# Optimization experiments

Measured on AMD Instinct MI355X. Metric: run time of the kernel, lower is better.

## Reference

```python
import jax, jax.numpy as jnp
import numpy as np

H = 512  # hidden_size

def setup_inputs() -> dict:
    key = jax.random.key(0)
    ks = jax.random.split(key, 5)
    B, S = 2, 512
    feats = jax.random.normal(ks[0], (B, S, H), dtype=jnp.float32)
    # torch Linear init ~ U(-1/sqrt(in), 1/sqrt(in)); scaled normals are fine for a reference
    W1 = jax.random.normal(ks[1], (2 * H, H), dtype=jnp.float32) / np.sqrt(2 * H)
    b1 = jnp.zeros((H,), dtype=jnp.float32)
    W2 = jax.random.normal(ks[2], (H, H // 2), dtype=jnp.float32) / np.sqrt(H)
    b2 = jnp.zeros((H // 2,), dtype=jnp.float32)
    W3 = jax.random.normal(ks[3], (H // 2, 1), dtype=jnp.float32) / np.sqrt(H // 2)
    b3 = jnp.zeros((1,), dtype=jnp.float32)
    return {"features": feats, "W1": W1, "b1": b1, "W2": W2, "b2": b2, "W3": W3, "b3": b3}


def reference(features, W1, b1, W2, b2, W3, b3):
    # cat([f_i, f_j]) @ W1 == f_i @ W1[:H] + f_j @ W1[H:]
    # Precompute the two halves once per residue instead of per pair.
    a = jnp.einsum('bsh,hk->bsk', features, W1[:H])          # [B,S,H]
    c = jnp.einsum('bsh,hk->bsk', features, W1[H:])          # [B,S,H]
    h1 = jax.nn.relu(a[:, :, None, :] + c[:, None, :, :] + b1)  # [B,S,S,H]
    # Dropout(0.1) is identity at inference.
    h2 = jax.nn.relu(jnp.einsum('bijh,hk->bijk', h1, W2) + b2)  # [B,S,S,H//2]
    logits = jnp.einsum('bijk,ko->bijo', h2, W3) + b3            # [B,S,S,1]
    return jax.nn.sigmoid(logits[..., 0])                        # [B,S,S]
```

## Files before the change

kernel.cpp:

```cpp
#include <hip/hip_runtime.h>

#define S_DIM 512
#define H_DIM 512
#define NH 256
#define TI 8
#define TJ 8

#define AS1 __attribute__((address_space(1)))
#define AS3 __attribute__((address_space(3)))

typedef _Float16 half8 __attribute__((ext_vector_type(8)));
typedef _Float16 half4 __attribute__((ext_vector_type(4)));
typedef float f32x4 __attribute__((ext_vector_type(4)));

__device__ __forceinline__ int swz(int r) { return ((r & 1) << 2) | (r >> 1); }

__global__ __launch_bounds__(256) void convert_all_kernel(const float* __restrict__ feats,
        const float* __restrict__ W1, const float* __restrict__ W2,
        _Float16* __restrict__ f16, _Float16* __restrict__ w1L, _Float16* __restrict__ w2L) {
    int blk = blockIdx.x;
    if (blk < 512) {
        int t = blk * 256 + threadIdx.x;
        float4 v = ((const float4*)feats)[t];
        half4 h;
        h.x = (_Float16)v.x; h.y = (_Float16)v.y; h.z = (_Float16)v.z; h.w = (_Float16)v.w;
        ((half4*)f16)[t] = h;
    } else if (blk < 768) {
        int t = (blk - 512) * 256 + threadIdx.x;
        int gcb = t >> 10, n = t & 1023;
        const float* src = (n < H_DIM) ? &W1[(size_t)(gcb * 8) * H_DIM + n]
                                       : &W1[(size_t)(H_DIM + gcb * 8) * H_DIM + (n - H_DIM)];
        half8 v;
#pragma unroll
        for (int j = 0; j < 8; j++) v[j] = (_Float16)src[(size_t)j * H_DIM];
        *(half8*)&w1L[((size_t)gcb * 1024 + n) * 8] = v;
    } else {
        int t = (blk - 768) * 256 + threadIdx.x;
        int gcb = t >> 8, n = t & 255;
        half8 v;
#pragma unroll
        for (int j = 0; j < 8; j++) v[j] = (_Float16)W2[(size_t)(gcb * 8 + j) * NH + n];
        *(half8*)&w2L[((size_t)gcb * 256 + n) * 8] = v;
    }
}

__global__ __launch_bounds__(256) void prep_mfma_kernel(const _Float16* __restrict__ f16,
        const _Float16* __restrict__ w1L, const float* __restrict__ b1,
        _Float16* __restrict__ aH, _Float16* __restrict__ cH) {
    const int n0 = blockIdx.x * 64, m0 = blockIdx.y * 64;
    const int tid = threadIdx.x, wave = tid >> 6, lane = tid & 63;
    const int quad = lane >> 4, l16 = lane & 15;
    const int wm = wave >> 1, wn = wave & 1;
    int mrow[2], ncol[2];
#pragma unroll
    for (int mt = 0; mt < 2; mt++) mrow[mt] = m0 + wm * 32 + mt * 16 + l16;
#pragma unroll
    for (int nt = 0; nt < 2; nt++) ncol[nt] = n0 + wn * 32 + nt * 16 + l16;
    f32x4 acc[2][2];
#pragma unroll
    for (int mt = 0; mt < 2; mt++)
#pragma unroll
        for (int nt = 0; nt < 2; nt++) acc[mt][nt] = (f32x4)0.f;
#pragma unroll
    for (int ks = 0; ks < 16; ks++) {
        int gcb = ks * 4 + quad;
        half8 af[2], bf[2];
#pragma unroll
        for (int mt = 0; mt < 2; mt++)
            af[mt] = *(const half8*)&f16[(size_t)mrow[mt] * H_DIM + gcb * 8];
#pragma unroll
        for (int nt = 0; nt < 2; nt++)
            bf[nt] = *(const half8*)&w1L[((size_t)gcb * 1024 + ncol[nt]) * 8];
#pragma unroll
        for (int nt = 0; nt < 2; nt++)
#pragma unroll
            for (int mt = 0; mt < 2; mt++)
                acc[mt][nt] = __builtin_amdgcn_mfma_f32_16x16x32_f16(af[mt], bf[nt],
                                                                     acc[mt][nt], 0, 0, 0);
    }
    const bool first_half = (n0 < H_DIM);
#pragma unroll
    for (int nt = 0; nt < 2; nt++) {
        float bias = first_half ? b1[ncol[nt]] : 0.f;
#pragma unroll
        for (int mt = 0; mt < 2; mt++)
#pragma unroll
            for (int r = 0; r < 4; r++) {
                int m = m0 + wm * 32 + mt * 16 + quad * 4 + r;
                float v = acc[mt][nt][r] + bias;
                if (first_half) aH[(size_t)m * H_DIM + ncol[nt]] = (_Float16)v;
                else            cH[(size_t)m * H_DIM + (ncol[nt] - H_DIM)] = (_Float16)v;
            }
    }
}

__global__ __launch_bounds__(256, 4) void pair_kernel(
        const _Float16* __restrict__ aH, const _Float16* __restrict__ cH,
        const _Float16* __restrict__ w2L,
        const float* __restrict__ b2, const float* __restrict__ W3,
        const float* __restrict__ b3, float* __restrict__ out) {
    const int jt = blockIdx.x, it = blockIdx.y, b = blockIdx.z;
    const int i0 = it * TI, j0 = jt * TJ;

    __shared__ __align__(16) _Float16 sa[TI * H_DIM];
    __shared__ __align__(16) _Float16 sc[TJ * H_DIM];
    __shared__ __align__(16) _Float16 afb[2][2][4][512];
    __shared__ float spart[4][64];

    const int tid = threadIdx.x;
    const int wave = tid >> 6, lane = tid & 63;
    const int quad = lane >> 4, l16 = lane & 15;
    const int nb = wave * 64;

#pragma unroll
    for (int rr0 = 0; rr0 < 2; rr0++) {
        int rr = rr0 * 4 + wave;
        int gc = lane ^ swz(rr & 7);
        __builtin_amdgcn_global_load_lds(
            (const AS1 unsigned int*)&aH[((size_t)(b * S_DIM + i0 + rr)) * H_DIM + gc * 8],
            (AS3 unsigned int*)&sa[rr * H_DIM], 16, 0, 0);
        __builtin_amdgcn_global_load_lds(
            (const AS1 unsigned int*)&cH[((size_t)(b * S_DIM + j0 + rr)) * H_DIM + gc * 8],
            (AS3 unsigned int*)&sc[rr * H_DIM], 16, 0, 0);
    }

    const int hl = l16 >> 3;
    const int ilW = wave * 2 + hl;
    const int saoffW = ilW * H_DIM;
    const int swzAW = swz(ilW);
    const int jl = l16 & 7;
    const int scoff = jl * H_DIM, swzC = swz(jl);

    f32x4 acc[4][4];
#pragma unroll
    for (int mt = 0; mt < 4; mt++)
#pragma unroll
        for (int nt = 0; nt < 4; nt++) acc[mt][nt] = (f32x4)0.f;

    const _Float16* bp = &w2L[((size_t)quad * 256 + nb + l16) * 8];

    half8 bnxt[4];
#pragma unroll
    for (int nt = 0; nt < 4; nt++) bnxt[nt] = *(const half8*)&bp[nt * 16 * 8];

    __syncthreads();

#pragma unroll
    for (int s = 0; s < 2; s++) {
        const int gcb = s * 4 + quad;
        half8 va = *(const half8*)&sa[saoffW + ((gcb ^ swzAW) * 8)];
        half8 vc = *(const half8*)&sc[scoff + ((gcb ^ swzC) * 8)];
        half8 af = __builtin_elementwise_max(va + vc, (half8)(_Float16)0.f);
        *(half8*)&afb[0][s][wave][lane * 8] = af;
    }
    asm volatile("s_waitcnt lgkmcnt(0)" ::: "memory");
    __builtin_amdgcn_s_barrier();
    __builtin_amdgcn_sched_barrier(0);

#pragma unroll
    for (int e = 0; e < 8; e++) {
        const int buf = e & 1;
#pragma unroll
        for (int s = 0; s < 2; s++) {
            const int ks = e * 2 + s;
            half8 bf[4];
#pragma unroll
            for (int nt = 0; nt < 4; nt++) bf[nt] = bnxt[nt];
            if (ks < 15) {
                const _Float16* bn = bp + (size_t)4 * 256 * 8;
#pragma unroll
                for (int nt = 0; nt < 4; nt++) bnxt[nt] = *(const half8*)&bn[nt * 16 * 8];
                bp = bn;
            }
            if (e < 7) {
                const int gcb = (2 * (e + 1) + s) * 4 + quad;
                half8 va = *(const half8*)&sa[saoffW + ((gcb ^ swzAW) * 8)];
                half8 vc = *(const half8*)&sc[scoff + ((gcb ^ swzC) * 8)];
                half8 af = __builtin_elementwise_max(va + vc, (half8)(_Float16)0.f);
                *(half8*)&afb[buf ^ 1][s][wave][lane * 8] = af;
            }
            half8 afr[4];
#pragma unroll
            for (int mt = 0; mt < 4; mt++)
                afr[mt] = *(const half8*)&afb[buf][s][mt][lane * 8];
            __builtin_amdgcn_s_setprio(1);
#pragma unroll
            for (int nt = 0; nt < 4; nt++)
#pragma unroll
                for (int mt = 0; mt < 4; mt++)
                    acc[mt][nt] = __builtin_amdgcn_mfma_f32_16x16x32_f16(afr[mt], bf[nt],
                                                                         acc[mt][nt], 0, 0, 0);
            __builtin_amdgcn_s_setprio(0);
        }
        if (e < 7) {
            asm volatile("s_waitcnt lgkmcnt(0)" ::: "memory");
            __builtin_amdgcn_s_barrier();
            __builtin_amdgcn_sched_barrier(0);
        }
    }

    float b2v[4], w3v[4];
#pragma unroll
    for (int nt = 0; nt < 4; nt++) {
        int n = nb + nt * 16 + l16;
        b2v[nt] = b2[n];
        w3v[nt] = W3[n];
    }
    float ps[4][4];
#pragma unroll
    for (int mt = 0; mt < 4; mt++)
#pragma unroll
        for (int r = 0; r < 4; r++) {
            float s = 0.f;
#pragma unroll
            for (int nt = 0; nt < 4; nt++) {
                float v = acc[mt][nt][r] + b2v[nt];
                v = v > 0.f ? v : 0.f;
                s += v * w3v[nt];
            }
            ps[mt][r] = s;
        }
#pragma unroll
    for (int mt = 0; mt < 4; mt++)
#pragma unroll
        for (int r = 0; r < 4; r++) {
            float s = ps[mt][r];
            s += __shfl_xor(s, 8, 16);
            s += __shfl_xor(s, 4, 16);
            s += __shfl_xor(s, 2, 16);
            s += __shfl_xor(s, 1, 16);
            ps[mt][r] = s;
        }
    if (l16 == 0) {
#pragma unroll
        for (int mt = 0; mt < 4; mt++)
#pragma unroll
            for (int r = 0; r < 4; r++)
                spart[wave][mt * 16 + quad * 4 + r] = ps[mt][r];
    }
    __syncthreads();
    if (tid < 64) {
        float tot = spart[0][tid] + spart[1][tid] + spart[2][tid] + spart[3][tid] + b3[0];
        float sg = 1.f / (1.f + __expf(-tot));
        int i = i0 + (tid >> 3), j = j0 + (tid & 7);
        out[(size_t)b * S_DIM * S_DIM + (size_t)i * S_DIM + j] = sg;
    }
}

extern "C" void kernel_launch(void* const* d_in, const int* in_sizes, int n_in,
                              void* d_out, int out_size, void* d_ws, size_t ws_size,
                              hipStream_t stream) {
    const float* feats = (const float*)d_in[0];
    const float* W1 = (const float*)d_in[1];
    const float* b1 = (const float*)d_in[2];
    const float* W2 = (const float*)d_in[3];
    const float* b2 = (const float*)d_in[4];
    const float* W3 = (const float*)d_in[5];
    const float* b3 = (const float*)d_in[6];
    float* out = (float*)d_out;

    const int B = in_sizes[0] / (S_DIM * H_DIM);
    const int M = B * S_DIM;

    char* ws = (char*)d_ws;
    _Float16* f16  = (_Float16*)ws;
    _Float16* aH   = (_Float16*)(ws + (1 << 20));
    _Float16* cH   = (_Float16*)(ws + (2 << 20));
    _Float16* w1L  = (_Float16*)(ws + (3 << 20));
    _Float16* w2L  = (_Float16*)(ws + (4 << 20));

    convert_all_kernel<<<832, 256, 0, stream>>>(feats, W1, W2, f16, w1L, w2L);
    prep_mfma_kernel<<<dim3(16, M / 64), 256, 0, stream>>>(f16, w1L, b1, aH, cH);
    pair_kernel<<<dim3(S_DIM / TJ, S_DIM / TI, B), 256, 0, stream>>>(aH, cH, w2L, b2, W3, b3, out);
}
```

Before: 203.9 us.

## Fuse three kernels into one persistent kernel with software grid barriers

Merges the convert, first-layer GEMM and pair kernels into a single persistent kernel of 768 blocks. The stages are separated by atomic-counter grid barriers, and the pair tiles are processed in a grid-stride loop. This is meant to remove two kernel launch gaps and their tail effects. In exchange it adds a memset, two grid-wide spins, and an occupancy hint lowered to 3, and the barrier relies on all 768 blocks being co-resident, which risks deadlock. The persistent loop also loses per-block scheduling flexibility.

```diff
diff --git a/kernel.cpp b/kernel.cpp
--- a/kernel.cpp
+++ b/kernel.cpp
@@ -5,6 +5,7 @@
 #define NH 256
 #define TI 8
 #define TJ 8
+#define NBLK 768
 
 #define AS1 __attribute__((address_space(1)))
 #define AS3 __attribute__((address_space(3)))
@@ -15,92 +16,27 @@
 
 __device__ __forceinline__ int swz(int r) { return ((r & 1) << 2) | (r >> 1); }
 
-__global__ __launch_bounds__(256) void convert_all_kernel(const float* __restrict__ feats,
-        const float* __restrict__ W1, const float* __restrict__ W2,
-        _Float16* __restrict__ f16, _Float16* __restrict__ w1L, _Float16* __restrict__ w2L) {
-    int blk = blockIdx.x;
-    if (blk < 512) {
-        int t = blk * 256 + threadIdx.x;
-        float4 v = ((const float4*)feats)[t];
-        half4 h;
-        h.x = (_Float16)v.x; h.y = (_Float16)v.y; h.z = (_Float16)v.z; h.w = (_Float16)v.w;
-        ((half4*)f16)[t] = h;
-    } else if (blk < 768) {
-        int t = (blk - 512) * 256 + threadIdx.x;
-        int gcb = t >> 10, n = t & 1023;
-        const float* src = (n < H_DIM) ? &W1[(size_t)(gcb * 8) * H_DIM + n]
-                                       : &W1[(size_t)(H_DIM + gcb * 8) * H_DIM + (n - H_DIM)];
-        half8 v;
-#pragma unroll
-        for (int j = 0; j < 8; j++) v[j] = (_Float16)src[(size_t)j * H_DIM];
-        *(half8*)&w1L[((size_t)gcb * 1024 + n) * 8] = v;
-    } else {
-        int t = (blk - 768) * 256 + threadIdx.x;
-        int gcb = t >> 8, n = t & 255;
-        half8 v;
-#pragma unroll
-        for (int j = 0; j < 8; j++) v[j] = (_Float16)W2[(size_t)(gcb * 8 + j) * NH + n];
-        *(half8*)&w2L[((size_t)gcb * 256 + n) * 8] = v;
-    }
+__device__ __forceinline__ void grid_barrier(unsigned* cnt) {
+    __syncthreads();
+    if (threadIdx.x == 0) {
+        __threadfence();
+        unsigned my = atomicAdd(cnt, 1u) + 1;
+        unsigned target = ((my + NBLK - 1) / NBLK) * NBLK;
+        while (__hip_atomic_load(cnt, __ATOMIC_RELAXED, __HIP_MEMORY_SCOPE_AGENT) < target)
+            __builtin_amdgcn_s_sleep(2);
+        __threadfence();
+    }
+    __syncthreads();
 }
 
-__global__ __launch_bounds__(256) void prep_mfma_kernel(const _Float16* __restrict__ f16,
-        const _Float16* __restrict__ w1L, const float* __restrict__ b1,
-        _Float16* __restrict__ aH, _Float16* __restrict__ cH) {
-    const int n0 = blockIdx.x * 64, m0 = blockIdx.y * 64;
-    const int tid = threadIdx.x, wave = tid >> 6, lane = tid & 63;
-    const int quad = lane >> 4, l16 = lane & 15;
-    const int wm = wave >> 1, wn = wave & 1;
-    int mrow[2], ncol[2];
-#pragma unroll
-    for (int mt = 0; mt < 2; mt++) mrow[mt] = m0 + wm * 32 + mt * 16 + l16;
-#pragma unroll
-    for (int nt = 0; nt < 2; nt++) ncol[nt] = n0 + wn * 32 + nt * 16 + l16;
-    f32x4 acc[2][2];
-#pragma unroll
-    for (int mt = 0; mt < 2; mt++)
-#pragma unroll
-        for (int nt = 0; nt < 2; nt++) acc[mt][nt] = (f32x4)0.f;
-#pragma unroll
-    for (int ks = 0; ks < 16; ks++) {
-        int gcb = ks * 4 + quad;
-        half8 af[2], bf[2];
-#pragma unroll
-        for (int mt = 0; mt < 2; mt++)
-            af[mt] = *(const half8*)&f16[(size_t)mrow[mt] * H_DIM + gcb * 8];
-#pragma unroll
-        for (int nt = 0; nt < 2; nt++)
-            bf[nt] = *(const half8*)&w1L[((size_t)gcb * 1024 + ncol[nt]) * 8];
-#pragma unroll
-        for (int nt = 0; nt < 2; nt++)
-#pragma unroll
-            for (int mt = 0; mt < 2; mt++)
-                acc[mt][nt] = __builtin_amdgcn_mfma_f32_16x16x32_f16(af[mt], bf[nt],
-                                                                     acc[mt][nt], 0, 0, 0);
-    }
-    const bool first_half = (n0 < H_DIM);
-#pragma unroll
-    for (int nt = 0; nt < 2; nt++) {
-        float bias = first_half ? b1[ncol[nt]] : 0.f;
-#pragma unroll
-        for (int mt = 0; mt < 2; mt++)
-#pragma unroll
-            for (int r = 0; r < 4; r++) {
-                int m = m0 + wm * 32 + mt * 16 + quad * 4 + r;
-                float v = acc[mt][nt][r] + bias;
-                if (first_half) aH[(size_t)m * H_DIM + ncol[nt]] = (_Float16)v;
-                else            cH[(size_t)m * H_DIM + (ncol[nt] - H_DIM)] = (_Float16)v;
-            }
-    }
-}
-
-__global__ __launch_bounds__(256, 4) void pair_kernel(
-        const _Float16* __restrict__ aH, const _Float16* __restrict__ cH,
-        const _Float16* __restrict__ w2L,
+__global__ __launch_bounds__(256, 3) void fused_kernel(
+        const float* __restrict__ feats, const float* __restrict__ W1,
+        const float* __restrict__ b1, const float* __restrict__ W2,
         const float* __restrict__ b2, const float* __restrict__ W3,
-        const float* __restrict__ b3, float* __restrict__ out) {
-    const int jt = blockIdx.x, it = blockIdx.y, b = blockIdx.z;
-    const int i0 = it * TI, j0 = jt * TJ;
+        const float* __restrict__ b3,
+        _Float16* __restrict__ f16, _Float16* __restrict__ w1L, _Float16* __restrict__ w2L,
+        _Float16* __restrict__ aH, _Float16* __restrict__ cH,
+        float* __restrict__ out, unsigned* __restrict__ cnt) {
 
     __shared__ __align__(16) _Float16 sa[TI * H_DIM];
     __shared__ __align__(16) _Float16 sc[TJ * H_DIM];
@@ -108,22 +44,88 @@
     __shared__ float spart[4][64];
 
     const int tid = threadIdx.x;
+
+    for (int u = blockIdx.x; u < 832; u += NBLK) {
+        if (u < 512) {
+            int t = u * 256 + tid;
+            float4 v = ((const float4*)feats)[t];
+            half4 h;
+            h.x = (_Float16)v.x; h.y = (_Float16)v.y; h.z = (_Float16)v.z; h.w = (_Float16)v.w;
+            ((half4*)f16)[t] = h;
+        } else if (u < 768) {
+            int t = (u - 512) * 256 + tid;
+            int gcb = t >> 10, n = t & 1023;
+            const float* src = (n < H_DIM) ? &W1[(size_t)(gcb * 8) * H_DIM + n]
+                                           : &W1[(size_t)(H_DIM + gcb * 8) * H_DIM + (n - H_DIM)];
+            half8 v;
+#pragma unroll
+            for (int j = 0; j < 8; j++) v[j] = (_Float16)src[(size_t)j * H_DIM];
+            *(half8*)&w1L[((size_t)gcb * 1024 + n) * 8] = v;
+        } else {
+            int t = (u - 768) * 256 + tid;
+            int gcb = t >> 8, n = t & 255;
+            half8 v;
+#pragma unroll
+            for (int j = 0; j < 8; j++) v[j] = (_Float16)W2[(size_t)(gcb * 8 + j) * NH + n];
+            *(half8*)&w2L[((size_t)gcb * 256 + n) * 8] = v;
+        }
+    }
+
+    grid_barrier(cnt);
+
+    for (int u = blockIdx.x; u < 256; u += NBLK) {
+        const int n0 = (u & 15) * 64, m0 = (u >> 4) * 64;
+        const int wave = tid >> 6, lane = tid & 63;
+        const int quad = lane >> 4, l16 = lane & 15;
+        const int wm = wave >> 1, wn = wave & 1;
+        int mrow[2], ncol[2];
+#pragma unroll
+        for (int mt = 0; mt < 2; mt++) mrow[mt] = m0 + wm * 32 + mt * 16 + l16;
+#pragma unroll
+        for (int nt = 0; nt < 2; nt++) ncol[nt] = n0 + wn * 32 + nt * 16 + l16;
+        f32x4 acc[2][2];
+#pragma unroll
+        for (int mt = 0; mt < 2; mt++)
+#pragma unroll
+            for (int nt = 0; nt < 2; nt++) acc[mt][nt] = (f32x4)0.f;
+#pragma unroll
+        for (int ks = 0; ks < 16; ks++) {
+            int gcb = ks * 4 + quad;
+            half8 af[2], bf[2];
+#pragma unroll
+            for (int mt = 0; mt < 2; mt++)
+                af[mt] = *(const half8*)&f16[(size_t)mrow[mt] * H_DIM + gcb * 8];
+#pragma unroll
+            for (int nt = 0; nt < 2; nt++)
+                bf[nt] = *(const half8*)&w1L[((size_t)gcb * 1024 + ncol[nt]) * 8];
+#pragma unroll
+            for (int nt = 0; nt < 2; nt++)
+#pragma unroll
+                for (int mt = 0; mt < 2; mt++)
+                    acc[mt][nt] = __builtin_amdgcn_mfma_f32_16x16x32_f16(af[mt], bf[nt],
+                                                                         acc[mt][nt], 0, 0, 0);
+        }
+        const bool first_half = (n0 < H_DIM);
+#pragma unroll
+        for (int nt = 0; nt < 2; nt++) {
+            float bias = first_half ? b1[ncol[nt]] : 0.f;
+#pragma unroll
+            for (int mt = 0; mt < 2; mt++)
+#pragma unroll
+                for (int r = 0; r < 4; r++) {
+                    int m = m0 + wm * 32 + mt * 16 + quad * 4 + r;
+                    float v = acc[mt][nt][r] + bias;
+                    if (first_half) aH[(size_t)m * H_DIM + ncol[nt]] = (_Float16)v;
+                    else            cH[(size_t)m * H_DIM + (ncol[nt] - H_DIM)] = (_Float16)v;
+                }
+        }
+    }
+
+    grid_barrier(cnt);
+
     const int wave = tid >> 6, lane = tid & 63;
     const int quad = lane >> 4, l16 = lane & 15;
     const int nb = wave * 64;
-
-#pragma unroll
-    for (int rr0 = 0; rr0 < 2; rr0++) {
-        int rr = rr0 * 4 + wave;
-        int gc = lane ^ swz(rr & 7);
-        __builtin_amdgcn_global_load_lds(
-            (const AS1 unsigned int*)&aH[((size_t)(b * S_DIM + i0 + rr)) * H_DIM + gc * 8],
-            (AS3 unsigned int*)&sa[rr * H_DIM], 16, 0, 0);
-        __builtin_amdgcn_global_load_lds(
-            (const AS1 unsigned int*)&cH[((size_t)(b * S_DIM + j0 + rr)) * H_DIM + gc * 8],
-            (AS3 unsigned int*)&sc[rr * H_DIM], 16, 0, 0);
-    }
-
     const int hl = l16 >> 3;
     const int ilW = wave * 2 + hl;
     const int saoffW = ilW * H_DIM;
@@ -131,119 +133,136 @@
     const int jl = l16 & 7;
     const int scoff = jl * H_DIM, swzC = swz(jl);
 
-    f32x4 acc[4][4];
-#pragma unroll
-    for (int mt = 0; mt < 4; mt++)
-#pragma unroll
-        for (int nt = 0; nt < 4; nt++) acc[mt][nt] = (f32x4)0.f;
-
-    const _Float16* bp = &w2L[((size_t)quad * 256 + nb + l16) * 8];
-
-    half8 bnxt[4];
-#pragma unroll
-    for (int nt = 0; nt < 4; nt++) bnxt[nt] = *(const half8*)&bp[nt * 16 * 8];
-
-    __syncthreads();
-
-#pragma unroll
-    for (int s = 0; s < 2; s++) {
-        const int gcb = s * 4 + quad;
-        half8 va = *(const half8*)&sa[saoffW + ((gcb ^ swzAW) * 8)];
-        half8 vc = *(const half8*)&sc[scoff + ((gcb ^ swzC) * 8)];
-        half8 af = __builtin_elementwise_max(va + vc, (half8)(_Float16)0.f);
-        *(half8*)&afb[0][s][wave][lane * 8] = af;
-    }
-    asm volatile("s_waitcnt lgkmcnt(0)" ::: "memory");
-    __builtin_amdgcn_s_barrier();
-    __builtin_amdgcn_sched_barrier(0);
-
-#pragma unroll
-    for (int e = 0; e < 8; e++) {
-        const int buf = e & 1;
+    for (int t = blockIdx.x; t < 64 * 64 * 2; t += NBLK) {
+        const int jt = t & 63, it = (t >> 6) & 63, b = t >> 12;
+        const int i0 = it * TI, j0 = jt * TJ;
+
+#pragma unroll
+        for (int rr0 = 0; rr0 < 2; rr0++) {
+            int rr = rr0 * 4 + wave;
+            int gc = lane ^ swz(rr & 7);
+            __builtin_amdgcn_global_load_lds(
+                (const AS1 unsigned int*)&aH[((size_t)(b * S_DIM + i0 + rr)) * H_DIM + gc * 8],
+                (AS3 unsigned int*)&sa[rr * H_DIM], 16, 0, 0);
+            __builtin_amdgcn_global_load_lds(
+                (const AS1 unsigned int*)&cH[((size_t)(b * S_DIM + j0 + rr)) * H_DIM + gc * 8],
+                (AS3 unsigned int*)&sc[rr * H_DIM], 16, 0, 0);
+        }
+
+        f32x4 acc[4][4];
+#pragma unroll
+        for (int mt = 0; mt < 4; mt++)
+#pragma unroll
+            for (int nt = 0; nt < 4; nt++) acc[mt][nt] = (f32x4)0.f;
+
+        const _Float16* bp = &w2L[((size_t)quad * 256 + nb + l16) * 8];
+        half8 bnxt[4];
+#pragma unroll
+        for (int nt = 0; nt < 4; nt++) bnxt[nt] = *(const half8*)&bp[nt * 16 * 8];
+
+        __syncthreads();
+
 #pragma unroll
         for (int s = 0; s < 2; s++) {
-            const int ks = e * 2 + s;
-            half8 bf[4];
-#pragma unroll
-            for (int nt = 0; nt < 4; nt++) bf[nt] = bnxt[nt];
-            if (ks < 15) {
-                const _Float16* bn = bp + (size_t)4 * 256 * 8;
-#pragma unroll
-                for (int nt = 0; nt < 4; nt++) bnxt[nt] = *(const half8*)&bn[nt * 16 * 8];
-                bp = bn;
+            const int gcb = s * 4 + quad;
+            half8 va = *(const half8*)&sa[saoffW + ((gcb ^ swzAW) * 8)];
+            half8 vc = *(const half8*)&sc[scoff + ((gcb ^ swzC) * 8)];
+            half8 af = __builtin_elementwise_max(va + vc, (half8)(_Float16)0.f);
+            *(half8*)&afb[0][s][wave][lane * 8] = af;
+        }
+        asm volatile("s_waitcnt lgkmcnt(0)" ::: "memory");
+        __builtin_amdgcn_s_barrier();
+        __builtin_amdgcn_sched_barrier(0);
+
+#pragma unroll
+        for (int e = 0; e < 8; e++) {
+            const int buf = e & 1;
+#pragma unroll
+            for (int s = 0; s < 2; s++) {
+                const int ks = e * 2 + s;
+                half8 bf[4];
+#pragma unroll
+                for (int nt = 0; nt < 4; nt++) bf[nt] = bnxt[nt];
+                if (ks < 15) {
+                    const _Float16* bn = bp + (size_t)4 * 256 * 8;
+#pragma unroll
+                    for (int nt = 0; nt < 4; nt++) bnxt[nt] = *(const half8*)&bn[nt * 16 * 8];
+                    bp = bn;
+                }
+                if (e < 7) {
+                    const int gcb = (2 * (e + 1) + s) * 4 + quad;
+                    half8 va = *(const half8*)&sa[saoffW + ((gcb ^ swzAW) * 8)];
+                    half8 vc = *(const half8*)&sc[scoff + ((gcb ^ swzC) * 8)];
+                    half8 af = __builtin_elementwise_max(va + vc, (half8)(_Float16)0.f);
+                    *(half8*)&afb[buf ^ 1][s][wave][lane * 8] = af;
+                }
+                half8 afr[4];
+#pragma unroll
+                for (int mt = 0; mt < 4; mt++)
+                    afr[mt] = *(const half8*)&afb[buf][s][mt][lane * 8];
+                __builtin_amdgcn_s_setprio(1);
+#pragma unroll
+                for (int nt = 0; nt < 4; nt++)
+#pragma unroll
+                    for (int mt = 0; mt < 4; mt++)
+                        acc[mt][nt] = __builtin_amdgcn_mfma_f32_16x16x32_f16(afr[mt], bf[nt],
+                                                                             acc[mt][nt], 0, 0, 0);
+                __builtin_amdgcn_s_setprio(0);
             }
             if (e < 7) {
-                const int gcb = (2 * (e + 1) + s) * 4 + quad;
-                half8 va = *(const half8*)&sa[saoffW + ((gcb ^ swzAW) * 8)];
-                half8 vc = *(const half8*)&sc[scoff + ((gcb ^ swzC) * 8)];
-                half8 af = __builtin_elementwise_max(va + vc, (half8)(_Float16)0.f);
-                *(half8*)&afb[buf ^ 1][s][wave][lane * 8] = af;
-            }
-            half8 afr[4];
+                asm volatile("s_waitcnt lgkmcnt(0)" ::: "memory");
+                __builtin_amdgcn_s_barrier();
+                __builtin_amdgcn_sched_barrier(0);
+            }
+        }
+
+        float b2v[4], w3v[4];
+#pragma unroll
+        for (int nt = 0; nt < 4; nt++) {
+            int n = nb + nt * 16 + l16;
+            b2v[nt] = b2[n];
+            w3v[nt] = W3[n];
+        }
+        float ps[4][4];
+#pragma unroll
+        for (int mt = 0; mt < 4; mt++)
+#pragma unroll
+            for (int r = 0; r < 4; r++) {
+                float s = 0.f;
+#pragma unroll
+                for (int nt = 0; nt < 4; nt++) {
+                    float v = acc[mt][nt][r] + b2v[nt];
+                    v = v > 0.f ? v : 0.f;
+                    s += v * w3v[nt];
+                }
+                ps[mt][r] = s;
+            }
+#pragma unroll
+        for (int mt = 0; mt < 4; mt++)
+#pragma unroll
+            for (int r = 0; r < 4; r++) {
+                float s = ps[mt][r];
+                s += __shfl_xor(s, 8, 16);
+                s += __shfl_xor(s, 4, 16);
+                s += __shfl_xor(s, 2, 16);
+                s += __shfl_xor(s, 1, 16);
+                ps[mt][r] = s;
+            }
+        if (l16 == 0) {
 #pragma unroll
             for (int mt = 0; mt < 4; mt++)
-                afr[mt] = *(const half8*)&afb[buf][s][mt][lane * 8];
-            __builtin_amdgcn_s_setprio(1);
-#pragma unroll
-            for (int nt = 0; nt < 4; nt++)
-#pragma unroll
-                for (int mt = 0; mt < 4; mt++)
-                    acc[mt][nt] = __builtin_amdgcn_mfma_f32_16x16x32_f16(afr[mt], bf[nt],
-                                                                         acc[mt][nt], 0, 0, 0);
-            __builtin_amdgcn_s_setprio(0);
-        }
-        if (e < 7) {
-            asm volatile("s_waitcnt lgkmcnt(0)" ::: "memory");
-            __builtin_amdgcn_s_barrier();
-            __builtin_amdgcn_sched_barrier(0);
-        }
-    }
-
-    float b2v[4], w3v[4];
-#pragma unroll
-    for (int nt = 0; nt < 4; nt++) {
-        int n = nb + nt * 16 + l16;
-        b2v[nt] = b2[n];
-        w3v[nt] = W3[n];
-    }
-    float ps[4][4];
-#pragma unroll
-    for (int mt = 0; mt < 4; mt++)
-#pragma unroll
-        for (int r = 0; r < 4; r++) {
-            float s = 0.f;
-#pragma unroll
-            for (int nt = 0; nt < 4; nt++) {
-                float v = acc[mt][nt][r] + b2v[nt];
-                v = v > 0.f ? v : 0.f;
-                s += v * w3v[nt];
-            }
-            ps[mt][r] = s;
-        }
-#pragma unroll
-    for (int mt = 0; mt < 4; mt++)
-#pragma unroll
-        for (int r = 0; r < 4; r++) {
-            float s = ps[mt][r];
-            s += __shfl_xor(s, 8, 16);
-            s += __shfl_xor(s, 4, 16);
-            s += __shfl_xor(s, 2, 16);
-            s += __shfl_xor(s, 1, 16);
-            ps[mt][r] = s;
-        }
-    if (l16 == 0) {
-#pragma unroll
-        for (int mt = 0; mt < 4; mt++)
-#pragma unroll
-            for (int r = 0; r < 4; r++)
-                spart[wave][mt * 16 + quad * 4 + r] = ps[mt][r];
-    }
-    __syncthreads();
-    if (tid < 64) {
-        float tot = spart[0][tid] + spart[1][tid] + spart[2][tid] + spart[3][tid] + b3[0];
-        float sg = 1.f / (1.f + __expf(-tot));
-        int i = i0 + (tid >> 3), j = j0 + (tid & 7);
-        out[(size_t)b * S_DIM * S_DIM + (size_t)i * S_DIM + j] = sg;
+#pragma unroll
+                for (int r = 0; r < 4; r++)
+                    spart[wave][mt * 16 + quad * 4 + r] = ps[mt][r];
+        }
+        __syncthreads();
+        if (tid < 64) {
+            float tot = spart[0][tid] + spart[1][tid] + spart[2][tid] + spart[3][tid] + b3[0];
+            float sg = 1.f / (1.f + __expf(-tot));
+            int i = i0 + (tid >> 3), j = j0 + (tid & 7);
+            out[(size_t)b * S_DIM * S_DIM + (size_t)i * S_DIM + j] = sg;
+        }
+        __syncthreads();
     }
 }
 
@@ -259,17 +278,15 @@
     const float* b3 = (const float*)d_in[6];
     float* out = (float*)d_out;
 
-    const int B = in_sizes[0] / (S_DIM * H_DIM);
-    const int M = B * S_DIM;
-
     char* ws = (char*)d_ws;
     _Float16* f16  = (_Float16*)ws;
     _Float16* aH   = (_Float16*)(ws + (1 << 20));
     _Float16* cH   = (_Float16*)(ws + (2 << 20));
     _Float16* w1L  = (_Float16*)(ws + (3 << 20));
     _Float16* w2L  = (_Float16*)(ws + (4 << 20));
-
-    convert_all_kernel<<<832, 256, 0, stream>>>(feats, W1, W2, f16, w1L, w2L);
-    prep_mfma_kernel<<<dim3(16, M / 64), 256, 0, stream>>>(f16, w1L, b1, aH, cH);
-    pair_kernel<<<dim3(S_DIM / TJ, S_DIM / TI, B), 256, 0, stream>>>(aH, cH, w2L, b2, W3, b3, out);
+    unsigned* cnt  = (unsigned*)(ws + (4 << 20) + (256 << 10));
+
+    hipMemsetAsync(cnt, 0, 16, stream);
+    fused_kernel<<<NBLK, 256, 0, stream>>>(feats, W1, b1, W2, b2, W3, b3,
+                                           f16, w1L, w2L, aH, cH, out, cnt);
 }
```

After: 606.1 us. 2.97x slower.

## Fuse fp32-to-fp16 conversion into projection GEMM and drop conversion kernel

Applied to the files above, without the earlier changes.

The separate conversion kernel and the projection GEMM are merged into one kernel. It reads fp32 features and W1 directly, converts them in registers, and transposes W1 tiles through shared memory. The W2 relayout blocks are appended to the same grid, which removes one launch and the fp16 intermediate buffers. In exchange the GEMM tiles shrink to 32 rows, so each block does less reuse, pays two barriers per k-step, and every block converts W1 again.

```diff
diff --git a/kernel.cpp b/kernel.cpp
--- a/kernel.cpp
+++ b/kernel.cpp
@@ -10,87 +10,88 @@
 #define AS3 __attribute__((address_space(3)))
 
 typedef _Float16 half8 __attribute__((ext_vector_type(8)));
-typedef _Float16 half4 __attribute__((ext_vector_type(4)));
 typedef float f32x4 __attribute__((ext_vector_type(4)));
 
 __device__ __forceinline__ int swz(int r) { return ((r & 1) << 2) | (r >> 1); }
 
-__global__ __launch_bounds__(256) void convert_all_kernel(const float* __restrict__ feats,
-        const float* __restrict__ W1, const float* __restrict__ W2,
-        _Float16* __restrict__ f16, _Float16* __restrict__ w1L, _Float16* __restrict__ w2L) {
-    int blk = blockIdx.x;
-    if (blk < 512) {
-        int t = blk * 256 + threadIdx.x;
-        float4 v = ((const float4*)feats)[t];
-        half4 h;
-        h.x = (_Float16)v.x; h.y = (_Float16)v.y; h.z = (_Float16)v.z; h.w = (_Float16)v.w;
-        ((half4*)f16)[t] = h;
-    } else if (blk < 768) {
-        int t = (blk - 512) * 256 + threadIdx.x;
-        int gcb = t >> 10, n = t & 1023;
-        const float* src = (n < H_DIM) ? &W1[(size_t)(gcb * 8) * H_DIM + n]
-                                       : &W1[(size_t)(H_DIM + gcb * 8) * H_DIM + (n - H_DIM)];
-        half8 v;
-#pragma unroll
-        for (int j = 0; j < 8; j++) v[j] = (_Float16)src[(size_t)j * H_DIM];
-        *(half8*)&w1L[((size_t)gcb * 1024 + n) * 8] = v;
-    } else {
-        int t = (blk - 768) * 256 + threadIdx.x;
+__global__ __launch_bounds__(256) void prep_fused_kernel(
+        const float* __restrict__ feats, const float* __restrict__ W1,
+        const float* __restrict__ b1, const float* __restrict__ W2,
+        _Float16* __restrict__ aH, _Float16* __restrict__ cH,
+        _Float16* __restrict__ w2L, int mblocks) {
+    const int tid = threadIdx.x;
+    const int blk = blockIdx.x;
+
+    if (blk >= 16 * mblocks) {
+        int t = (blk - 16 * mblocks) * 256 + tid;
         int gcb = t >> 8, n = t & 255;
         half8 v;
 #pragma unroll
         for (int j = 0; j < 8; j++) v[j] = (_Float16)W2[(size_t)(gcb * 8 + j) * NH + n];
         *(half8*)&w2L[((size_t)gcb * 256 + n) * 8] = v;
-    }
-}
-
-__global__ __launch_bounds__(256) void prep_mfma_kernel(const _Float16* __restrict__ f16,
-        const _Float16* __restrict__ w1L, const float* __restrict__ b1,
-        _Float16* __restrict__ aH, _Float16* __restrict__ cH) {
-    const int n0 = blockIdx.x * 64, m0 = blockIdx.y * 64;
-    const int tid = threadIdx.x, wave = tid >> 6, lane = tid & 63;
+        return;
+    }
+
+    __shared__ __align__(16) _Float16 sw1T[64][40];
+
+    const int n0 = (blk & 15) * 64, m0 = (blk >> 4) * 32;
+    const int wave = tid >> 6, lane = tid & 63;
     const int quad = lane >> 4, l16 = lane & 15;
     const int wm = wave >> 1, wn = wave & 1;
-    int mrow[2], ncol[2];
-#pragma unroll
-    for (int mt = 0; mt < 2; mt++) mrow[mt] = m0 + wm * 32 + mt * 16 + l16;
+
+    const int mrow = m0 + wm * 16 + l16;
+    int ncol[2];
 #pragma unroll
     for (int nt = 0; nt < 2; nt++) ncol[nt] = n0 + wn * 32 + nt * 16 + l16;
-    f32x4 acc[2][2];
-#pragma unroll
-    for (int mt = 0; mt < 2; mt++)
-#pragma unroll
-        for (int nt = 0; nt < 2; nt++) acc[mt][nt] = (f32x4)0.f;
-#pragma unroll
+
+    const bool first_half = (n0 < H_DIM);
+    const int rbase = first_half ? 0 : H_DIM;
+    const int cbase = first_half ? n0 : (n0 - H_DIM);
+
+    const int n4 = tid & 15, hh = tid >> 4;
+
+    f32x4 acc[2];
+#pragma unroll
+    for (int nt = 0; nt < 2; nt++) acc[nt] = (f32x4)0.f;
+
     for (int ks = 0; ks < 16; ks++) {
-        int gcb = ks * 4 + quad;
-        half8 af[2], bf[2];
-#pragma unroll
-        for (int mt = 0; mt < 2; mt++)
-            af[mt] = *(const half8*)&f16[(size_t)mrow[mt] * H_DIM + gcb * 8];
+        __syncthreads();
+        const float* wsrc = &W1[(size_t)(rbase + ks * 32) * H_DIM + cbase];
+#pragma unroll
+        for (int p = 0; p < 2; p++) {
+            float4 v = *(const float4*)&wsrc[(size_t)(hh + p * 16) * H_DIM + n4 * 4];
+            sw1T[n4 * 4 + 0][hh + p * 16] = (_Float16)v.x;
+            sw1T[n4 * 4 + 1][hh + p * 16] = (_Float16)v.y;
+            sw1T[n4 * 4 + 2][hh + p * 16] = (_Float16)v.z;
+            sw1T[n4 * 4 + 3][hh + p * 16] = (_Float16)v.w;
+        }
+        __syncthreads();
+        const float* fp = &feats[(size_t)mrow * H_DIM + ks * 32 + quad * 8];
+        float4 a0 = ((const float4*)fp)[0], a1 = ((const float4*)fp)[1];
+        half8 af;
+        af[0] = (_Float16)a0.x; af[1] = (_Float16)a0.y;
+        af[2] = (_Float16)a0.z; af[3] = (_Float16)a0.w;
+        af[4] = (_Float16)a1.x; af[5] = (_Float16)a1.y;
+        af[6] = (_Float16)a1.z; af[7] = (_Float16)a1.w;
+        half8 bf[2];
 #pragma unroll
         for (int nt = 0; nt < 2; nt++)
-            bf[nt] = *(const half8*)&w1L[((size_t)gcb * 1024 + ncol[nt]) * 8];
+            bf[nt] = *(const half8*)&sw1T[wn * 32 + nt * 16 + l16][quad * 8];
 #pragma unroll
         for (int nt = 0; nt < 2; nt++)
-#pragma unroll
-            for (int mt = 0; mt < 2; mt++)
-                acc[mt][nt] = __builtin_amdgcn_mfma_f32_16x16x32_f16(af[mt], bf[nt],
-                                                                     acc[mt][nt], 0, 0, 0);
-    }
-    const bool first_half = (n0 < H_DIM);
+            acc[nt] = __builtin_amdgcn_mfma_f32_16x16x32_f16(af, bf[nt], acc[nt], 0, 0, 0);
+    }
+
 #pragma unroll
     for (int nt = 0; nt < 2; nt++) {
         float bias = first_half ? b1[ncol[nt]] : 0.f;
 #pragma unroll
-        for (int mt = 0; mt < 2; mt++)
-#pragma unroll
-            for (int r = 0; r < 4; r++) {
-                int m = m0 + wm * 32 + mt * 16 + quad * 4 + r;
-                float v = acc[mt][nt][r] + bias;
-                if (first_half) aH[(size_t)m * H_DIM + ncol[nt]] = (_Float16)v;
-                else            cH[(size_t)m * H_DIM + (ncol[nt] - H_DIM)] = (_Float16)v;
-            }
+        for (int r = 0; r < 4; r++) {
+            int m = m0 + wm * 16 + quad * 4 + r;
+            float v = acc[nt][r] + bias;
+            if (first_half) aH[(size_t)m * H_DIM + ncol[nt]] = (_Float16)v;
+            else            cH[(size_t)m * H_DIM + (ncol[nt] - H_DIM)] = (_Float16)v;
+        }
     }
 }
 
@@ -261,15 +262,14 @@
 
     const int B = in_sizes[0] / (S_DIM * H_DIM);
     const int M = B * S_DIM;
+    const int mblocks = M / 32;
 
     char* ws = (char*)d_ws;
-    _Float16* f16  = (_Float16*)ws;
-    _Float16* aH   = (_Float16*)(ws + (1 << 20));
-    _Float16* cH   = (_Float16*)(ws + (2 << 20));
-    _Float16* w1L  = (_Float16*)(ws + (3 << 20));
-    _Float16* w2L  = (_Float16*)(ws + (4 << 20));
-
-    convert_all_kernel<<<832, 256, 0, stream>>>(feats, W1, W2, f16, w1L, w2L);
-    prep_mfma_kernel<<<dim3(16, M / 64), 256, 0, stream>>>(f16, w1L, b1, aH, cH);
+    _Float16* aH   = (_Float16*)ws;
+    _Float16* cH   = (_Float16*)(ws + (1 << 20));
+    _Float16* w2L  = (_Float16*)(ws + (2 << 20));
+
+    prep_fused_kernel<<<16 * mblocks + 64, 256, 0, stream>>>(feats, W1, b1, W2,
+                                                             aH, cH, w2L, mblocks);
     pair_kernel<<<dim3(S_DIM / TJ, S_DIM / TI, B), 256, 0, stream>>>(aH, cH, w2L, b2, W3, b3, out);
 }
```

After: 203.9 us. No clear change (-0.0%).
